# Kernel tuning notes

Measured on AMD Instinct MI355X. Metric: run time of the kernel, lower is better.

The kernel has to match this reference:

```python
import jax, jax.numpy as jnp
import numpy as np

N, T, D, H = 64, 512, 1024, 1024


def setup_inputs() -> dict:
    key = jax.random.key(0)
    k1, k2, k3, k4 = jax.random.split(key, 4)
    x = jax.random.normal(k1, (N, T, D), dtype=jnp.float32)
    h0 = jax.random.normal(k2, (N, H), dtype=jnp.float32)
    Wx = jax.random.normal(k3, (D, 4 * H), dtype=jnp.float32) / np.sqrt(D)
    Wh = jax.random.normal(k4, (H, 4 * H), dtype=jnp.float32) / np.sqrt(H)
    b = jnp.zeros((4 * H,), dtype=jnp.float32)
    return {"x": x, "h0": h0, "Wx": Wx, "Wh": Wh, "b": b}


def lstm_scan(x, h0, Wx, Wh, b):
    # Precompute input projection for all timesteps in one big GEMM: (N,T,4H)
    xW = jnp.einsum('ntd,dg->ntg', x, Wx) + b
    Hdim = h0.shape[1]
    c0 = jnp.zeros_like(h0)

    def step(carry, xw_t):
        prev_h, prev_c = carry
        a = xw_t + prev_h @ Wh  # (N, 4H)
        i = jax.nn.sigmoid(a[:, :Hdim])
        f = jax.nn.sigmoid(a[:, Hdim:2 * Hdim])
        o = jax.nn.sigmoid(a[:, 2 * Hdim:3 * Hdim])
        g = jnp.tanh(a[:, 3 * Hdim:])
        next_c = f * prev_c + i * g
        next_h = o * jnp.tanh(next_c)
        return (next_h, next_c), next_h

    # scan over time axis: move T to leading dim
    _, hs = jax.lax.scan(step, (h0, c0), jnp.swapaxes(xW, 0, 1))
    return jnp.swapaxes(hs, 0, 1)  # (N, T, H)


def reference(x, h0, Wx, Wh, b):
    return lstm_scan(x, h0, Wx, Wh, b)
```

## Files before the change

### kernel.cpp

```cpp
#include <hip/hip_runtime.h>
#include <hip/hip_bf16.h>
#include <cmath>

typedef __attribute__((ext_vector_type(8))) short short8;
typedef __attribute__((ext_vector_type(4))) float floatx4;

#define TS   512
#define DIM  1024
#define HD   1024
#define KTOT 2048
#define GRID_BLOCKS 256
#define XSTRIDE 1032
#define ROWSTRIDE ((size_t)TS * HD)

__global__ void build_wt(const float* __restrict__ Wx,
                         const float* __restrict__ Wh,
                         __hip_bfloat16* __restrict__ WT) {
    __shared__ __hip_bfloat16 tile[32][33];
    const int j0 = blockIdx.x * 32;
    const int k0 = blockIdx.y * 32;
    const int tx = threadIdx.x & 31;
    const int ty = threadIdx.x >> 5;
    #pragma unroll
    for (int kk = 0; kk < 32; kk += 8) {
        const int k = k0 + ty + kk;
        const float* S = (k < DIM) ? (Wx + (size_t)k * 4096)
                                   : (Wh + (size_t)(k - DIM) * 4096);
        tile[ty + kk][tx] = __float2bfloat16(S[j0 + tx]);
    }
    __syncthreads();
    #pragma unroll
    for (int kk = 0; kk < 32; kk += 8) {
        const int j = j0 + ty + kk;
        WT[(size_t)j * KTOT + k0 + tx] = tile[tx][ty + kk];
    }
}

__global__ __launch_bounds__(256, 1)
void lstm_scan(const float* __restrict__ x,
               const float* __restrict__ h0,
               const __hip_bfloat16* __restrict__ WT,
               const float* __restrict__ bias,
               float* __restrict__ out,
               unsigned* __restrict__ hbuf32) {
    __shared__ __hip_bfloat16 XB[2][16][XSTRIDE];
    __shared__ __hip_bfloat16 Bh[16][XSTRIDE];
    __shared__ float lds_g[4][16][17];

    const int blk  = blockIdx.x;
    const int ng   = (blk >> 1) & 3;
    const int cs   = ((blk >> 3) << 1) | (blk & 1);
    const int tid  = threadIdx.x;
    const int wave = tid >> 6;
    const int lane = tid & 63;
    const int n0 = ng * 16;
    const int j0 = cs * 16;

    const int frag_m = lane & 15;
    const int frag_k = (lane >> 4) * 8;

    const int flat = blk * 256 + tid;
    {
        const unsigned w0 =
            ((unsigned)(unsigned short)__bfloat16_as_short(__float2bfloat16(h0[flat])) << 16) | 1u;
        __hip_atomic_store(hbuf32 + flat, w0,
                           __ATOMIC_RELAXED, __HIP_MEMORY_SCOPE_AGENT);
    }

    const __hip_bfloat16* wrow =
        WT + (size_t)(wave * HD + j0 + frag_m) * KTOT + frag_k;
    short8 wreg[64];
    #pragma unroll
    for (int i = 0; i < 32; ++i)
        wreg[i] = *(const short8*)(wrow + i * 32);
    #pragma unroll
    for (int i = 0; i < 32; ++i)
        wreg[32 + i] = *(const short8*)(wrow + DIM + i * 32);

    #pragma unroll
    for (int j = 0; j < 8; ++j) {
        const int c = j * 256 + tid;
        const int r = c >> 7;
        const int col = (c & 127) * 8;
        const float* xs = x + (size_t)(n0 + r) * ROWSTRIDE + col;
        float4 f0 = *(const float4*)xs;
        float4 f1 = *(const float4*)(xs + 4);
        short8 v;
        v[0] = __bfloat16_as_short(__float2bfloat16(f0.x));
        v[1] = __bfloat16_as_short(__float2bfloat16(f0.y));
        v[2] = __bfloat16_as_short(__float2bfloat16(f0.z));
        v[3] = __bfloat16_as_short(__float2bfloat16(f0.w));
        v[4] = __bfloat16_as_short(__float2bfloat16(f1.x));
        v[5] = __bfloat16_as_short(__float2bfloat16(f1.y));
        v[6] = __bfloat16_as_short(__float2bfloat16(f1.z));
        v[7] = __bfloat16_as_short(__float2bfloat16(f1.w));
        *(short8*)&XB[0][r][col] = v;
    }

    const int e_j = tid & 15;
    const int e_n = tid >> 4;
    float c_reg = 0.0f;
    const float bi  = bias[         j0 + e_j];
    const float bf_ = bias[1 * HD + j0 + e_j];
    const float bo  = bias[2 * HD + j0 + e_j];
    const float bg  = bias[3 * HD + j0 + e_j];
    float* out_e = out + (size_t)(n0 + e_n) * ROWSTRIDE + j0 + e_j;
    const int hb_idx = (n0 + e_n) * 1024 + j0 + e_j;
    const int q = lane >> 4;

    for (int t = 0; t < TS; ++t) {
        const int par = t & 1;

        float4 xf[16];
        if (t + 1 < TS) {
            #pragma unroll
            for (int j = 0; j < 8; ++j) {
                const int c = j * 256 + tid;
                const int r = c >> 7;
                const int col = (c & 127) * 8;
                const float* xs = x + (size_t)(n0 + r) * ROWSTRIDE
                                    + (size_t)(t + 1) * DIM + col;
                xf[2 * j]     = *(const float4*)xs;
                xf[2 * j + 1] = *(const float4*)(xs + 4);
            }
        }

        unsigned long long hb[32];
        const unsigned long long* pb =
            (const unsigned long long*)hbuf32 + ((size_t)par << 15);
        const unsigned long long tagpat =
            (unsigned long long)(unsigned)(t + 1)
            | ((unsigned long long)(unsigned)(t + 1) << 32);
        bool ok;
        do {
            ok = true;
            #pragma unroll
            for (int j = 0; j < 8; ++j) {
                const int c = j * 256 + tid;
                const int r = c >> 7;
                const int col = (c & 127) * 8;
                const size_t o = (size_t)(((n0 + r) << 10) + col) >> 1;
                #pragma unroll
                for (int qq = 0; qq < 4; ++qq)
                    hb[4 * j + qq] = __hip_atomic_load(pb + o + qq,
                        __ATOMIC_RELAXED, __HIP_MEMORY_SCOPE_AGENT);
            }
            #pragma unroll
            for (int k = 0; k < 32; ++k)
                ok = ok && ((hb[k] & 0x0000FFFF0000FFFFull) == tagpat);
        } while (!__all((int)ok));

        #pragma unroll
        for (int j = 0; j < 8; ++j) {
            const int c = j * 256 + tid;
            const int r = c >> 7;
            const int col = (c & 127) * 8;
            short8 v;
            #pragma unroll
            for (int qq = 0; qq < 4; ++qq) {
                const unsigned long long u = hb[4 * j + qq];
                v[2 * qq]     = (short)((unsigned)u >> 16);
                v[2 * qq + 1] = (short)(u >> 48);
            }
            *(short8*)&Bh[r][col] = v;
        }

        if (t + 1 < TS) {
            #pragma unroll
            for (int j = 0; j < 8; ++j) {
                const int c = j * 256 + tid;
                const int r = c >> 7;
                const int col = (c & 127) * 8;
                const float4 f0 = xf[2 * j];
                const float4 f1 = xf[2 * j + 1];
                short8 v;
                v[0] = __bfloat16_as_short(__float2bfloat16(f0.x));
                v[1] = __bfloat16_as_short(__float2bfloat16(f0.y));
                v[2] = __bfloat16_as_short(__float2bfloat16(f0.z));
                v[3] = __bfloat16_as_short(__float2bfloat16(f0.w));
                v[4] = __bfloat16_as_short(__float2bfloat16(f1.x));
                v[5] = __bfloat16_as_short(__float2bfloat16(f1.y));
                v[6] = __bfloat16_as_short(__float2bfloat16(f1.z));
                v[7] = __bfloat16_as_short(__float2bfloat16(f1.w));
                *(short8*)&XB[(t + 1) & 1][r][col] = v;
            }
        }
        __syncthreads();

        floatx4 a0 = {0.f, 0.f, 0.f, 0.f};
        floatx4 a1 = {0.f, 0.f, 0.f, 0.f};
        floatx4 a2 = {0.f, 0.f, 0.f, 0.f};
        floatx4 a3 = {0.f, 0.f, 0.f, 0.f};
        #pragma unroll
        for (int i = 0; i < 32; i += 2) {
            short8 b8a = *(const short8*)&XB[par][frag_m][i * 32 + frag_k];
            short8 b8b = *(const short8*)&XB[par][frag_m][(i + 1) * 32 + frag_k];
            a0 = __builtin_amdgcn_mfma_f32_16x16x32_bf16(wreg[i],     b8a, a0, 0, 0, 0);
            a1 = __builtin_amdgcn_mfma_f32_16x16x32_bf16(wreg[i + 1], b8b, a1, 0, 0, 0);
        }
        #pragma unroll
        for (int i = 0; i < 32; i += 2) {
            short8 b8a = *(const short8*)&Bh[frag_m][i * 32 + frag_k];
            short8 b8b = *(const short8*)&Bh[frag_m][(i + 1) * 32 + frag_k];
            a2 = __builtin_amdgcn_mfma_f32_16x16x32_bf16(wreg[32 + i], b8a, a2, 0, 0, 0);
            a3 = __builtin_amdgcn_mfma_f32_16x16x32_bf16(wreg[33 + i], b8b, a3, 0, 0, 0);
        }
        floatx4 acc = (a0 + a1) + (a2 + a3);

        #pragma unroll
        for (int r = 0; r < 4; ++r)
            lds_g[wave][q * 4 + r][frag_m] = acc[r];
        __syncthreads();

        const float ai = lds_g[0][e_j][e_n] + bi;
        const float af = lds_g[1][e_j][e_n] + bf_;
        const float ao = lds_g[2][e_j][e_n] + bo;
        const float ag = lds_g[3][e_j][e_n] + bg;
        const float i_g = 1.0f / (1.0f + expf(-ai));
        const float f_g = 1.0f / (1.0f + expf(-af));
        const float o_g = 1.0f / (1.0f + expf(-ao));
        const float g_g = tanhf(ag);
        c_reg = f_g * c_reg + i_g * g_g;
        const float h = o_g * tanhf(c_reg);

        if (t + 1 < TS) {
            const unsigned wrd =
                ((unsigned)(unsigned short)__bfloat16_as_short(__float2bfloat16(h)) << 16)
                | (unsigned)(t + 2);
            __hip_atomic_store(hbuf32 + (((size_t)((t + 1) & 1)) << 16) + hb_idx, wrd,
                               __ATOMIC_RELAXED, __HIP_MEMORY_SCOPE_AGENT);
        }

        out_e[(size_t)t * HD] = h;
    }
}

extern "C" void kernel_launch(void* const* d_in, const int* in_sizes, int n_in,
                              void* d_out, int out_size, void* d_ws, size_t ws_size,
                              hipStream_t stream) {
    const float* x  = (const float*)d_in[0];
    const float* h0 = (const float*)d_in[1];
    const float* Wx = (const float*)d_in[2];
    const float* Wh = (const float*)d_in[3];
    const float* b  = (const float*)d_in[4];
    float* out = (float*)d_out;

    char* ws = (char*)d_ws;
    __hip_bfloat16* WT     = (__hip_bfloat16*)ws;
    unsigned*       hbuf32 = (unsigned*)(ws + (16u << 20));

    hipMemsetAsync(hbuf32, 0, 2 * 65536 * sizeof(unsigned), stream);
    build_wt<<<dim3(128, 64), 256, 0, stream>>>(Wx, Wh, WT);
    lstm_scan<<<GRID_BLOCKS, 256, 0, stream>>>(x, h0, WT, b, out, hbuf32);
}
```

Baseline: 3.282 ms.

## Overlap input-projection MFMA with h spin-wait and chunk the recurrent h fetch

The x-projection MFMAs now run before the cross-block spin-wait on the previous hidden state, so they overlap with the wait on other blocks. The h fetch is split into four column chunks, each issued ahead of the MFMAs on the prior chunk, so load latency and waiting are pipelined with compute. Sigmoid and tanh switch to fast exp/rcp intrinsics, and the next x tile conversion moves after the gate math. In exchange the kernel adds more __syncthreads per step and loses a little precision in the activations.

```diff
diff --git a/kernel.cpp b/kernel.cpp
--- a/kernel.cpp
+++ b/kernel.cpp
@@ -34,6 +34,13 @@
         const int j = j0 + ty + kk;
         WT[(size_t)j * KTOT + k0 + tx] = tile[tx][ty + kk];
     }
+}
+
+__device__ __forceinline__ float fast_sig(float x) {
+    return __builtin_amdgcn_rcpf(1.0f + __expf(-x));
+}
+__device__ __forceinline__ float fast_tanh(float x) {
+    return 1.0f - 2.0f * __builtin_amdgcn_rcpf(1.0f + __expf(2.0f * x));
 }
 
 __global__ __launch_bounds__(256, 1)
@@ -96,6 +103,7 @@
         v[7] = __bfloat16_as_short(__float2bfloat16(f1.w));
         *(short8*)&XB[0][r][col] = v;
     }
+    __syncthreads();
 
     const int e_j = tid & 15;
     const int e_n = tid >> 4;
@@ -108,8 +116,12 @@
     const int hb_idx = (n0 + e_n) * 1024 + j0 + e_j;
     const int q = lane >> 4;
 
+    const int s_sl = tid & 31;
+    const int r1   = tid >> 5;
+
     for (int t = 0; t < TS; ++t) {
         const int par = t & 1;
+        const int nxt = (t + 1) & 1;
 
         float4 xf[16];
         if (t + 1 < TS) {
@@ -125,45 +137,110 @@
             }
         }
 
-        unsigned long long hb[32];
+        floatx4 a0 = {0.f, 0.f, 0.f, 0.f};
+        floatx4 a1 = {0.f, 0.f, 0.f, 0.f};
+        #pragma unroll
+        for (int i = 0; i < 32; i += 2) {
+            short8 b8a = *(const short8*)&XB[par][frag_m][i * 32 + frag_k];
+            short8 b8b = *(const short8*)&XB[par][frag_m][(i + 1) * 32 + frag_k];
+            a0 = __builtin_amdgcn_mfma_f32_16x16x32_bf16(wreg[i],     b8a, a0, 0, 0, 0);
+            a1 = __builtin_amdgcn_mfma_f32_16x16x32_bf16(wreg[i + 1], b8b, a1, 0, 0, 0);
+        }
+
         const unsigned long long* pb =
             (const unsigned long long*)hbuf32 + ((size_t)par << 15);
         const unsigned long long tagpat =
             (unsigned long long)(unsigned)(t + 1)
             | ((unsigned long long)(unsigned)(t + 1) << 32);
-        bool ok;
-        do {
-            ok = true;
-            #pragma unroll
-            for (int j = 0; j < 8; ++j) {
-                const int c = j * 256 + tid;
-                const int r = c >> 7;
-                const int col = (c & 127) * 8;
-                const size_t o = (size_t)(((n0 + r) << 10) + col) >> 1;
-                #pragma unroll
-                for (int qq = 0; qq < 4; ++qq)
-                    hb[4 * j + qq] = __hip_atomic_load(pb + o + qq,
-                        __ATOMIC_RELAXED, __HIP_MEMORY_SCOPE_AGENT);
-            }
-            #pragma unroll
-            for (int k = 0; k < 32; ++k)
-                ok = ok && ((hb[k] & 0x0000FFFF0000FFFFull) == tagpat);
-        } while (!__all((int)ok));
+        unsigned long long hb[8];
+        floatx4 a2 = {0.f, 0.f, 0.f, 0.f};
+        floatx4 a3 = {0.f, 0.f, 0.f, 0.f};
+
+#define ISSUE8(CC) do {                                                        \
+        const size_t o1 = ((size_t)(n0 + r1) << 9) + ((CC) << 7) + (s_sl << 2);\
+        _Pragma("unroll")                                                      \
+        for (int qq = 0; qq < 4; ++qq)                                         \
+            hb[qq] = __hip_atomic_load(pb + o1 + qq,                           \
+                __ATOMIC_RELAXED, __HIP_MEMORY_SCOPE_AGENT);                   \
+        _Pragma("unroll")                                                      \
+        for (int qq = 0; qq < 4; ++qq)                                         \
+            hb[4 + qq] = __hip_atomic_load(pb + o1 + (8 << 9) + qq,            \
+                __ATOMIC_RELAXED, __HIP_MEMORY_SCOPE_AGENT);                   \
+    } while (0)
+
+#define TAGOK() ({ bool ok_ = true;                                            \
+        _Pragma("unroll")                                                      \
+        for (int kk = 0; kk < 8; ++kk)                                         \
+            ok_ = ok_ && ((hb[kk] & 0x0000FFFF0000FFFFull) == tagpat);         \
+        ok_; })
+
+#define SPIN(CC) do { ISSUE8(CC); } while (!__all((int)TAGOK()))
+
+#define CHECKSPIN(CC) do { if (!__all((int)TAGOK())) { SPIN(CC); } } while (0)
+
+#define EXTRACT(CC) do {                                                       \
+        const int cb = (CC) * 256 + s_sl * 8;                                  \
+        short8 v0, v1;                                                         \
+        _Pragma("unroll")                                                      \
+        for (int qq = 0; qq < 4; ++qq) {                                       \
+            const unsigned long long u = hb[qq];                               \
+            v0[2 * qq]     = (short)(unsigned short)(u >> 16);                 \
+            v0[2 * qq + 1] = (short)(unsigned short)(u >> 48);                 \
+            const unsigned long long w = hb[4 + qq];                           \
+            v1[2 * qq]     = (short)(unsigned short)(w >> 16);                 \
+            v1[2 * qq + 1] = (short)(unsigned short)(w >> 48);                 \
+        }                                                                      \
+        *(short8*)&Bh[r1][cb]     = v0;                                        \
+        *(short8*)&Bh[r1 + 8][cb] = v1;                                        \
+    } while (0)
+
+#define HMFMA(CC) do {                                                         \
+        _Pragma("unroll")                                                      \
+        for (int k = 0; k < 8; k += 2) {                                       \
+            short8 b8a = *(const short8*)&Bh[frag_m][((CC)*8 + k)     * 32 + frag_k]; \
+            short8 b8b = *(const short8*)&Bh[frag_m][((CC)*8 + k + 1) * 32 + frag_k]; \
+            a2 = __builtin_amdgcn_mfma_f32_16x16x32_bf16(wreg[32 + (CC)*8 + k],     b8a, a2, 0, 0, 0); \
+            a3 = __builtin_amdgcn_mfma_f32_16x16x32_bf16(wreg[32 + (CC)*8 + k + 1], b8b, a3, 0, 0, 0); \
+        }                                                                      \
+    } while (0)
+
+        SPIN(0); EXTRACT(0);
+        __syncthreads();
+        ISSUE8(1); HMFMA(0); CHECKSPIN(1); EXTRACT(1);
+        __syncthreads();
+        ISSUE8(2); HMFMA(1); CHECKSPIN(2); EXTRACT(2);
+        __syncthreads();
+        ISSUE8(3); HMFMA(2); CHECKSPIN(3); EXTRACT(3);
+        __syncthreads();
+        HMFMA(3);
+
+        floatx4 acc = (a0 + a1) + (a2 + a3);
 
         #pragma unroll
-        for (int j = 0; j < 8; ++j) {
-            const int c = j * 256 + tid;
-            const int r = c >> 7;
-            const int col = (c & 127) * 8;
-            short8 v;
-            #pragma unroll
-            for (int qq = 0; qq < 4; ++qq) {
-                const unsigned long long u = hb[4 * j + qq];
-                v[2 * qq]     = (short)((unsigned)u >> 16);
-                v[2 * qq + 1] = (short)(u >> 48);
-            }
-            *(short8*)&Bh[r][col] = v;
-        }
+        for (int r = 0; r < 4; ++r)
+            lds_g[wave][q * 4 + r][frag_m] = acc[r];
+        __syncthreads();
+
+        const float ai = lds_g[0][e_j][e_n] + bi;
+        const float af = lds_g[1][e_j][e_n] + bf_;
+        const float ao = lds_g[2][e_j][e_n] + bo;
+        const float ag = lds_g[3][e_j][e_n] + bg;
+        const float i_g = fast_sig(ai);
+        const float f_g = fast_sig(af);
+        const float o_g = fast_sig(ao);
+        const float g_g = fast_tanh(ag);
+        c_reg = f_g * c_reg + i_g * g_g;
+        const float h = o_g * fast_tanh(c_reg);
+
+        if (t + 1 < TS) {
+            const unsigned wrd =
+                ((unsigned)(unsigned short)__bfloat16_as_short(__float2bfloat16(h)) << 16)
+                | (unsigned)(t + 2);
+            __hip_atomic_store(hbuf32 + (((size_t)nxt) << 16) + hb_idx, wrd,
+                               __ATOMIC_RELAXED, __HIP_MEMORY_SCOPE_AGENT);
+        }
+
+        out_e[(size_t)t * HD] = h;
 
         if (t + 1 < TS) {
             #pragma unroll
@@ -182,57 +259,17 @@
                 v[5] = __bfloat16_as_short(__float2bfloat16(f1.y));
                 v[6] = __bfloat16_as_short(__float2bfloat16(f1.z));
                 v[7] = __bfloat16_as_short(__float2bfloat16(f1.w));
-                *(short8*)&XB[(t + 1) & 1][r][col] = v;
+                *(short8*)&XB[nxt][r][col] = v;
             }
-        }
-        __syncthreads();
-
-        floatx4 a0 = {0.f, 0.f, 0.f, 0.f};
-        floatx4 a1 = {0.f, 0.f, 0.f, 0.f};
-        floatx4 a2 = {0.f, 0.f, 0.f, 0.f};
-        floatx4 a3 = {0.f, 0.f, 0.f, 0.f};
-        #pragma unroll
-        for (int i = 0; i < 32; i += 2) {
-            short8 b8a = *(const short8*)&XB[par][frag_m][i * 32 + frag_k];
-            short8 b8b = *(const short8*)&XB[par][frag_m][(i + 1) * 32 + frag_k];
-            a0 = __builtin_amdgcn_mfma_f32_16x16x32_bf16(wreg[i],     b8a, a0, 0, 0, 0);
-            a1 = __builtin_amdgcn_mfma_f32_16x16x32_bf16(wreg[i + 1], b8b, a1, 0, 0, 0);
-        }
-        #pragma unroll
-        for (int i = 0; i < 32; i += 2) {
-            short8 b8a = *(const short8*)&Bh[frag_m][i * 32 + frag_k];
-            short8 b8b = *(const short8*)&Bh[frag_m][(i + 1) * 32 + frag_k];
-            a2 = __builtin_amdgcn_mfma_f32_16x16x32_bf16(wreg[32 + i], b8a, a2, 0, 0, 0);
-            a3 = __builtin_amdgcn_mfma_f32_16x16x32_bf16(wreg[33 + i], b8b, a3, 0, 0, 0);
-        }
-        floatx4 acc = (a0 + a1) + (a2 + a3);
-
-        #pragma unroll
-        for (int r = 0; r < 4; ++r)
-            lds_g[wave][q * 4 + r][frag_m] = acc[r];
-        __syncthreads();
-
-        const float ai = lds_g[0][e_j][e_n] + bi;
-        const float af = lds_g[1][e_j][e_n] + bf_;
-        const float ao = lds_g[2][e_j][e_n] + bo;
-        const float ag = lds_g[3][e_j][e_n] + bg;
-        const float i_g = 1.0f / (1.0f + expf(-ai));
-        const float f_g = 1.0f / (1.0f + expf(-af));
-        const float o_g = 1.0f / (1.0f + expf(-ao));
-        const float g_g = tanhf(ag);
-        c_reg = f_g * c_reg + i_g * g_g;
-        const float h = o_g * tanhf(c_reg);
-
-        if (t + 1 < TS) {
-            const unsigned wrd =
-                ((unsigned)(unsigned short)__bfloat16_as_short(__float2bfloat16(h)) << 16)
-                | (unsigned)(t + 2);
-            __hip_atomic_store(hbuf32 + (((size_t)((t + 1) & 1)) << 16) + hb_idx, wrd,
-                               __ATOMIC_RELAXED, __HIP_MEMORY_SCOPE_AGENT);
-        }
-
-        out_e[(size_t)t * HD] = h;
-    }
+            __syncthreads();
+        }
+    }
+#undef ISSUE8
+#undef TAGOK
+#undef SPIN
+#undef CHECKSPIN
+#undef EXTRACT
+#undef HMFMA
 }
 
 extern "C" void kernel_launch(void* const* d_in, const int* in_sizes, int n_in,
```

Measured after the change: 4.410 ms. +34.4%, slower.

## Poll a single sentinel word before bulk h load, widen ring, use fast gates

Applied to the files above, without the earlier changes.

Each wave now spins on one tagged word per lane (with s_sleep) before issuing the full 32-qword hidden-state load, then re-reads only the entries whose tags are still stale. The h exchange buffer grows from a 2-slot to a 4-slot ring. Sigmoid and tanh switch to __expf plus hardware reciprocal. This is meant to cut polling memory traffic and per-step latency on the cross-block recurrence critical path, at some cost in activation accuracy. The non-atomic bulk load after the sentinel relies on tags for correctness.

```diff
diff --git a/kernel.cpp b/kernel.cpp
--- a/kernel.cpp
+++ b/kernel.cpp
@@ -10,6 +10,7 @@
 #define HD   1024
 #define KTOT 2048
 #define GRID_BLOCKS 256
+#define RING 4
 #define XSTRIDE 1032
 #define ROWSTRIDE ((size_t)TS * HD)
 
@@ -34,6 +35,13 @@
         const int j = j0 + ty + kk;
         WT[(size_t)j * KTOT + k0 + tx] = tile[tx][ty + kk];
     }
+}
+
+__device__ __forceinline__ float fast_sig(float x) {
+    return __builtin_amdgcn_rcpf(1.0f + __expf(-x));
+}
+__device__ __forceinline__ float fast_tanh(float x) {
+    return 1.0f - 2.0f * __builtin_amdgcn_rcpf(1.0f + __expf(2.0f * x));
 }
 
 __global__ __launch_bounds__(256, 1)
@@ -108,8 +116,12 @@
     const int hb_idx = (n0 + e_n) * 1024 + j0 + e_j;
     const int q = lane >> 4;
 
+    const unsigned c_idx =
+        (unsigned)((n0 + (lane & 15)) * 1024 + lane * 16 + (lane >> 4));
+
     for (int t = 0; t < TS; ++t) {
-        const int par = t & 1;
+        const int slot_r = t & (RING - 1);
+        const int slot_w = (t + 1) & (RING - 1);
 
         float4 xf[16];
         if (t + 1 < TS) {
@@ -125,15 +137,38 @@
             }
         }
 
+        const unsigned* pb32 = hbuf32 + ((size_t)slot_r << 16);
+        const unsigned tg = (unsigned)(t + 1);
+
+        for (;;) {
+            unsigned v = __hip_atomic_load(pb32 + c_idx,
+                __ATOMIC_RELAXED, __HIP_MEMORY_SCOPE_AGENT);
+            if (__all((int)((v & 0xFFFFu) == tg))) break;
+            __builtin_amdgcn_s_sleep(1);
+        }
+        asm volatile("" ::: "memory");
+
+        const unsigned long long* pb = (const unsigned long long*)pb32;
+        const unsigned long long tagpat =
+            (unsigned long long)tg | ((unsigned long long)tg << 32);
         unsigned long long hb[32];
-        const unsigned long long* pb =
-            (const unsigned long long*)hbuf32 + ((size_t)par << 15);
-        const unsigned long long tagpat =
-            (unsigned long long)(unsigned)(t + 1)
-            | ((unsigned long long)(unsigned)(t + 1) << 32);
-        bool ok;
-        do {
-            ok = true;
+        #pragma unroll
+        for (int j = 0; j < 8; ++j) {
+            const int c = j * 256 + tid;
+            const int r = c >> 7;
+            const int col = (c & 127) * 8;
+            const size_t o = (size_t)(((n0 + r) << 10) + col) >> 1;
+            #pragma unroll
+            for (int qq = 0; qq < 4; ++qq)
+                hb[4 * j + qq] = pb[o + qq];
+        }
+
+        for (;;) {
+            bool ok = true;
+            #pragma unroll
+            for (int k = 0; k < 32; ++k)
+                ok = ok && ((hb[k] & 0x0000FFFF0000FFFFull) == tagpat);
+            if (__all((int)ok)) break;
             #pragma unroll
             for (int j = 0; j < 8; ++j) {
                 const int c = j * 256 + tid;
@@ -142,13 +177,11 @@
                 const size_t o = (size_t)(((n0 + r) << 10) + col) >> 1;
                 #pragma unroll
                 for (int qq = 0; qq < 4; ++qq)
-                    hb[4 * j + qq] = __hip_atomic_load(pb + o + qq,
-                        __ATOMIC_RELAXED, __HIP_MEMORY_SCOPE_AGENT);
-            }
-            #pragma unroll
-            for (int k = 0; k < 32; ++k)
-                ok = ok && ((hb[k] & 0x0000FFFF0000FFFFull) == tagpat);
-        } while (!__all((int)ok));
+                    if ((hb[4 * j + qq] & 0x0000FFFF0000FFFFull) != tagpat)
+                        hb[4 * j + qq] = __hip_atomic_load(pb + o + qq,
+                            __ATOMIC_RELAXED, __HIP_MEMORY_SCOPE_AGENT);
+            }
+        }
 
         #pragma unroll
         for (int j = 0; j < 8; ++j) {
@@ -159,8 +192,8 @@
             #pragma unroll
             for (int qq = 0; qq < 4; ++qq) {
                 const unsigned long long u = hb[4 * j + qq];
-                v[2 * qq]     = (short)((unsigned)u >> 16);
-                v[2 * qq + 1] = (short)(u >> 48);
+                v[2 * qq]     = (short)(unsigned short)(u >> 16);
+                v[2 * qq + 1] = (short)(unsigned short)(u >> 48);
             }
             *(short8*)&Bh[r][col] = v;
         }
@@ -187,6 +220,7 @@
         }
         __syncthreads();
 
+        const int par = t & 1;
         floatx4 a0 = {0.f, 0.f, 0.f, 0.f};
         floatx4 a1 = {0.f, 0.f, 0.f, 0.f};
         floatx4 a2 = {0.f, 0.f, 0.f, 0.f};
@@ -216,18 +250,18 @@
         const float af = lds_g[1][e_j][e_n] + bf_;
         const float ao = lds_g[2][e_j][e_n] + bo;
         const float ag = lds_g[3][e_j][e_n] + bg;
-        const float i_g = 1.0f / (1.0f + expf(-ai));
-        const float f_g = 1.0f / (1.0f + expf(-af));
-        const float o_g = 1.0f / (1.0f + expf(-ao));
-        const float g_g = tanhf(ag);
+        const float i_g = fast_sig(ai);
+        const float f_g = fast_sig(af);
+        const float o_g = fast_sig(ao);
+        const float g_g = fast_tanh(ag);
         c_reg = f_g * c_reg + i_g * g_g;
-        const float h = o_g * tanhf(c_reg);
+        const float h = o_g * fast_tanh(c_reg);
 
         if (t + 1 < TS) {
             const unsigned wrd =
                 ((unsigned)(unsigned short)__bfloat16_as_short(__float2bfloat16(h)) << 16)
                 | (unsigned)(t + 2);
-            __hip_atomic_store(hbuf32 + (((size_t)((t + 1) & 1)) << 16) + hb_idx, wrd,
+            __hip_atomic_store(hbuf32 + (((size_t)slot_w) << 16) + hb_idx, wrd,
                                __ATOMIC_RELAXED, __HIP_MEMORY_SCOPE_AGENT);
         }
 
@@ -249,7 +283,7 @@
     __hip_bfloat16* WT     = (__hip_bfloat16*)ws;
     unsigned*       hbuf32 = (unsigned*)(ws + (16u << 20));
 
-    hipMemsetAsync(hbuf32, 0, 2 * 65536 * sizeof(unsigned), stream);
+    hipMemsetAsync(hbuf32, 0, RING * 65536 * sizeof(unsigned), stream);
     build_wt<<<dim3(128, 64), 256, 0, stream>>>(Wx, Wh, WT);
     lstm_scan<<<GRID_BLOCKS, 256, 0, stream>>>(x, h0, WT, b, out, hbuf32);
 }
```

After: 3.330 ms. About the same (+1.5%).

## Overlap x-projection MFMAs with h-flag spin and gate in registers

Applied to the files above, without the earlier changes.

Moves the x·Wx MFMA half ahead of the spin-wait on the previous timestep's hidden state, so input-projection work overlaps the cross-block synchronization latency. Reorders the weight rows so each wave owns four columns across all four gates, which lets gate values be redistributed with lane shuffles instead of an LDS round trip and a second __syncthreads. Double-buffers the Bh tile, which the removed barrier requires. Replaces expf/tanhf with rcp and fast exp approximations, trading a little accuracy for fewer instructions on the serial critical path.

```diff
diff --git a/kernel.cpp b/kernel.cpp
--- a/kernel.cpp
+++ b/kernel.cpp
@@ -36,6 +36,13 @@
     }
 }
 
+__device__ __forceinline__ float fast_sig(float x) {
+    return __builtin_amdgcn_rcpf(1.0f + __expf(-x));
+}
+__device__ __forceinline__ float fast_tanh(float x) {
+    return 1.0f - 2.0f * __builtin_amdgcn_rcpf(1.0f + __expf(2.0f * x));
+}
+
 __global__ __launch_bounds__(256, 1)
 void lstm_scan(const float* __restrict__ x,
                const float* __restrict__ h0,
@@ -44,8 +51,7 @@
                float* __restrict__ out,
                unsigned* __restrict__ hbuf32) {
     __shared__ __hip_bfloat16 XB[2][16][XSTRIDE];
-    __shared__ __hip_bfloat16 Bh[16][XSTRIDE];
-    __shared__ float lds_g[4][16][17];
+    __shared__ __hip_bfloat16 Bh[2][16][XSTRIDE];
 
     const int blk  = blockIdx.x;
     const int ng   = (blk >> 1) & 3;
@@ -58,6 +64,7 @@
 
     const int frag_m = lane & 15;
     const int frag_k = (lane >> 4) * 8;
+    const int q      = lane >> 4;
 
     const int flat = blk * 256 + tid;
     {
@@ -67,8 +74,8 @@
                            __ATOMIC_RELAXED, __HIP_MEMORY_SCOPE_AGENT);
     }
 
-    const __hip_bfloat16* wrow =
-        WT + (size_t)(wave * HD + j0 + frag_m) * KTOT + frag_k;
+    const int arow = ((frag_m >> 2) * HD) + j0 + 4 * wave + (frag_m & 3);
+    const __hip_bfloat16* wrow = WT + (size_t)arow * KTOT + frag_k;
     short8 wreg[64];
     #pragma unroll
     for (int i = 0; i < 32; ++i)
@@ -96,20 +103,21 @@
         v[7] = __bfloat16_as_short(__float2bfloat16(f1.w));
         *(short8*)&XB[0][r][col] = v;
     }
-
-    const int e_j = tid & 15;
-    const int e_n = tid >> 4;
+    __syncthreads();
+
+    const int jl = j0 + 4 * wave + q;
+    const int nl = n0 + frag_m;
     float c_reg = 0.0f;
-    const float bi  = bias[         j0 + e_j];
-    const float bf_ = bias[1 * HD + j0 + e_j];
-    const float bo  = bias[2 * HD + j0 + e_j];
-    const float bg  = bias[3 * HD + j0 + e_j];
-    float* out_e = out + (size_t)(n0 + e_n) * ROWSTRIDE + j0 + e_j;
-    const int hb_idx = (n0 + e_n) * 1024 + j0 + e_j;
-    const int q = lane >> 4;
+    const float bi  = bias[         jl];
+    const float bf_ = bias[1 * HD + jl];
+    const float bo  = bias[2 * HD + jl];
+    const float bg  = bias[3 * HD + jl];
+    float* out_e = out + (size_t)nl * ROWSTRIDE + jl;
+    const int hb_idx = nl * 1024 + jl;
 
     for (int t = 0; t < TS; ++t) {
         const int par = t & 1;
+        const int nxt = (t + 1) & 1;
 
         float4 xf[16];
         if (t + 1 < TS) {
@@ -125,12 +133,23 @@
             }
         }
 
-        unsigned long long hb[32];
+        floatx4 a0 = {0.f, 0.f, 0.f, 0.f};
+        floatx4 a1 = {0.f, 0.f, 0.f, 0.f};
+        #pragma unroll
+        for (int i = 0; i < 32; i += 2) {
+            short8 b8a = *(const short8*)&XB[par][frag_m][i * 32 + frag_k];
+            short8 b8b = *(const short8*)&XB[par][frag_m][(i + 1) * 32 + frag_k];
+            a0 = __builtin_amdgcn_mfma_f32_16x16x32_bf16(wreg[i],     b8a, a0, 0, 0, 0);
+            a1 = __builtin_amdgcn_mfma_f32_16x16x32_bf16(wreg[i + 1], b8b, a1, 0, 0, 0);
+        }
+        __builtin_amdgcn_sched_barrier(0);
+
         const unsigned long long* pb =
             (const unsigned long long*)hbuf32 + ((size_t)par << 15);
         const unsigned long long tagpat =
             (unsigned long long)(unsigned)(t + 1)
             | ((unsigned long long)(unsigned)(t + 1) << 32);
+        unsigned long long hb[32];
         bool ok;
         do {
             ok = true;
@@ -159,10 +178,10 @@
             #pragma unroll
             for (int qq = 0; qq < 4; ++qq) {
                 const unsigned long long u = hb[4 * j + qq];
-                v[2 * qq]     = (short)((unsigned)u >> 16);
-                v[2 * qq + 1] = (short)(u >> 48);
-            }
-            *(short8*)&Bh[r][col] = v;
+                v[2 * qq]     = (short)(unsigned short)(u >> 16);
+                v[2 * qq + 1] = (short)(unsigned short)(u >> 48);
+            }
+            *(short8*)&Bh[par][r][col] = v;
         }
 
         if (t + 1 < TS) {
@@ -182,52 +201,52 @@
                 v[5] = __bfloat16_as_short(__float2bfloat16(f1.y));
                 v[6] = __bfloat16_as_short(__float2bfloat16(f1.z));
                 v[7] = __bfloat16_as_short(__float2bfloat16(f1.w));
-                *(short8*)&XB[(t + 1) & 1][r][col] = v;
+                *(short8*)&XB[nxt][r][col] = v;
             }
         }
         __syncthreads();
 
-        floatx4 a0 = {0.f, 0.f, 0.f, 0.f};
-        floatx4 a1 = {0.f, 0.f, 0.f, 0.f};
         floatx4 a2 = {0.f, 0.f, 0.f, 0.f};
         floatx4 a3 = {0.f, 0.f, 0.f, 0.f};
         #pragma unroll
         for (int i = 0; i < 32; i += 2) {
-            short8 b8a = *(const short8*)&XB[par][frag_m][i * 32 + frag_k];
-            short8 b8b = *(const short8*)&XB[par][frag_m][(i + 1) * 32 + frag_k];
-            a0 = __builtin_amdgcn_mfma_f32_16x16x32_bf16(wreg[i],     b8a, a0, 0, 0, 0);
-            a1 = __builtin_amdgcn_mfma_f32_16x16x32_bf16(wreg[i + 1], b8b, a1, 0, 0, 0);
-        }
-        #pragma unroll
-        for (int i = 0; i < 32; i += 2) {
-            short8 b8a = *(const short8*)&Bh[frag_m][i * 32 + frag_k];
-            short8 b8b = *(const short8*)&Bh[frag_m][(i + 1) * 32 + frag_k];
+            short8 b8a = *(const short8*)&Bh[par][frag_m][i * 32 + frag_k];
+            short8 b8b = *(const short8*)&Bh[par][frag_m][(i + 1) * 32 + frag_k];
             a2 = __builtin_amdgcn_mfma_f32_16x16x32_bf16(wreg[32 + i], b8a, a2, 0, 0, 0);
             a3 = __builtin_amdgcn_mfma_f32_16x16x32_bf16(wreg[33 + i], b8b, a3, 0, 0, 0);
         }
         floatx4 acc = (a0 + a1) + (a2 + a3);
 
-        #pragma unroll
-        for (int r = 0; r < 4; ++r)
-            lds_g[wave][q * 4 + r][frag_m] = acc[r];
-        __syncthreads();
-
-        const float ai = lds_g[0][e_j][e_n] + bi;
-        const float af = lds_g[1][e_j][e_n] + bf_;
-        const float ao = lds_g[2][e_j][e_n] + bo;
-        const float ag = lds_g[3][e_j][e_n] + bg;
-        const float i_g = 1.0f / (1.0f + expf(-ai));
-        const float f_g = 1.0f / (1.0f + expf(-af));
-        const float o_g = 1.0f / (1.0f + expf(-ao));
-        const float g_g = tanhf(ag);
+        float a[4] = {acc[0], acc[1], acc[2], acc[3]};
+        {
+            float s0 = (q & 1) ? a[0] : a[1];
+            float r0 = __shfl_xor(s0, 16);
+            if (q & 1) a[0] = r0; else a[1] = r0;
+            float s1 = (q & 1) ? a[2] : a[3];
+            float r1 = __shfl_xor(s1, 16);
+            if (q & 1) a[2] = r1; else a[3] = r1;
+        }
+        {
+            float s0 = (q & 2) ? a[0] : a[2];
+            float r0 = __shfl_xor(s0, 32);
+            if (q & 2) a[0] = r0; else a[2] = r0;
+            float s1 = (q & 2) ? a[1] : a[3];
+            float r1 = __shfl_xor(s1, 32);
+            if (q & 2) a[1] = r1; else a[3] = r1;
+        }
+
+        const float i_g = fast_sig(a[0] + bi);
+        const float f_g = fast_sig(a[1] + bf_);
+        const float o_g = fast_sig(a[2] + bo);
+        const float g_g = fast_tanh(a[3] + bg);
         c_reg = f_g * c_reg + i_g * g_g;
-        const float h = o_g * tanhf(c_reg);
+        const float h = o_g * fast_tanh(c_reg);
 
         if (t + 1 < TS) {
             const unsigned wrd =
                 ((unsigned)(unsigned short)__bfloat16_as_short(__float2bfloat16(h)) << 16)
                 | (unsigned)(t + 2);
-            __hip_atomic_store(hbuf32 + (((size_t)((t + 1) & 1)) << 16) + hb_idx, wrd,
+            __hip_atomic_store(hbuf32 + (((size_t)nxt) << 16) + hb_idx, wrd,
                                __ATOMIC_RELAXED, __HIP_MEMORY_SCOPE_AGENT);
         }
 
```

Measured after the change: 3.706 ms. 1.13x slower.
